# Kernel tuning notes

Hardware: AMD Instinct MI355X
Metric: run time of the kernel (lower is better)

Reference implementation:

```python
import jax, jax.numpy as jnp
import numpy as np

B, N, C, H = 8, 4096, 768, 32
D = C // H  # head_dim = 24
EPS = 1e-12


def _l2norm(t):
    # F.normalize(dim=-1): t / max(||t||_2, eps)
    n = jnp.sqrt(jnp.sum(t * t, axis=-1, keepdims=True))
    return t / jnp.maximum(n, EPS)


def setup_inputs() -> dict:
    key = jax.random.key(0)
    ks = jax.random.split(key, 6)
    s_in = 1.0 / np.sqrt(C)
    return {
        "x": jax.random.normal(ks[0], (B, N, C), dtype=jnp.float32),
        "W_qkv": jax.random.uniform(ks[1], (C, 3 * C), jnp.float32, -s_in, s_in),
        "b_qkv": jax.random.uniform(ks[2], (3 * C,), jnp.float32, -s_in, s_in),
        "temperature": jnp.ones((H, 1, 1), dtype=jnp.float32),
        "W_proj": jax.random.uniform(ks[3], (C, C), jnp.float32, -s_in, s_in),
        "b_proj": jax.random.uniform(ks[4], (C,), jnp.float32, -s_in, s_in),
    }


def reference(x, W_qkv, b_qkv, temperature, W_proj, b_proj):
    b, n, c = x.shape
    qkv = x @ W_qkv + b_qkv                                  # (B,N,3C)
    qkv = qkv.reshape(b, n, 3, H, D).transpose(2, 0, 3, 1, 4)  # (3,B,H,N,D)
    q, k, v = qkv[0], qkv[1], qkv[2]                         # (B,H,N,D)
    q = jnp.swapaxes(q, -1, -2)                              # (B,H,D,N)
    k = jnp.swapaxes(k, -1, -2)
    v = jnp.swapaxes(v, -1, -2)
    q = _l2norm(q)                                           # normalize over N
    k = _l2norm(k)
    attn = jnp.einsum('bhdn,bhen->bhde', q, k) * temperature  # (B,H,D,D)
    attn = jax.nn.softmax(attn, axis=-1)
    y = jnp.einsum('bhde,bhen->bhdn', attn, v)               # (B,H,D,N)
    # Faithful to torch: (1,B,H,D,N).transpose(1,2).reshape(B,N,C)
    # == (H,B,D,N) flattened row-major into (B,N,C)
    y = jnp.transpose(y, (1, 0, 2, 3)).reshape(b, n, c)
    return y @ W_proj + b_proj
```

## Files before the change

### kernel.cpp

```cpp
#include <hip/hip_runtime.h>
#include <hip/hip_bf16.h>


#define DEVI __device__ __forceinline__

typedef __attribute__((ext_vector_type(8))) short bf16x8;
typedef __attribute__((ext_vector_type(4))) float f32x4;
typedef __attribute__((ext_vector_type(4))) unsigned int u32x4;
typedef unsigned int u32;
typedef unsigned short u16;

DEVI u16 f2bf(float f) {
  union { float f; u32 u; } x; x.f = f;
  u32 r = x.u + 0x7FFFu + ((x.u >> 16) & 1u);
  return (u16)(r >> 16);
}

DEVI u32 cvtpk(float a, float b) {
  u32 r;
  asm("v_cvt_pk_bf16_f32 %0, %1, %2" : "=v"(r) : "v"(a), "v"(b));
  return r;
}

DEVI void gload_lds16(const void* g, void* l) {
  __builtin_amdgcn_global_load_lds((__attribute__((address_space(1))) void*)g,
                                   (__attribute__((address_space(3))) void*)l, 16, 0, 0);
}

__global__ __launch_bounds__(256) void transpose_cvt(const float* __restrict__ W,
                                                     u16* __restrict__ Wt, int K, int N) {
  __shared__ float tile[32][33];
  int n0 = blockIdx.x * 32, k0 = blockIdx.y * 32;
  int tx = threadIdx.x, ty = threadIdx.y;
  #pragma unroll
  for (int i = 0; i < 4; ++i)
    tile[ty + 8 * i][tx] = W[(long)(k0 + ty + 8 * i) * N + n0 + tx];
  __syncthreads();
  #pragma unroll
  for (int i = 0; i < 4; ++i)
    Wt[(long)(n0 + ty + 8 * i) * K + k0 + tx] = f2bf(tile[tx][ty + 8 * i]);
}

template<int NT>
__global__ __launch_bounds__(512, 2) void gemm_k1f_kernel(
    const float* __restrict__ X, const u16* __restrict__ Bt,
    const float* __restrict__ bias, u16* __restrict__ Cout, int N) {
  constexpr int K = NT * 32;
  __shared__ __attribute__((aligned(128))) char lds[73728];

  int nbx = N >> 8;
  int nwg = gridDim.x;
  int bid = blockIdx.x;
  bid = (bid & 7) * (nwg >> 3) + (bid >> 3);
  int bx = bid % nbx, by = bid / nbx;

  int t = threadIdx.x;
  int w = t >> 6, l = t & 63;
  int wr = w >> 2, wc = w & 3;
  int l16 = l & 15, l4 = l >> 4;

  int cbb = (l4 * 16) ^ ((l16 & 8) << 2);
  int pA0 = (wr * 64 + l16) * 64 + cbb;
  int pB0 = (wc * 64 + l16) * 64 + cbb;

  int pa = t * 16;
  int la = pa ^ (((pa >> 9) & 1) << 5);
  int soffA = (la >> 6) * K + ((la & 63) >> 1);
  int soffB[2];
  #pragma unroll
  for (int j = 0; j < 2; ++j) {
    int p = (j * 512 + t) * 16;
    int lb = p ^ (((p >> 9) & 1) << 5);
    soffB[j] = (lb >> 6) * K + ((lb & 63) >> 1);
  }

  const float* Ag = X + (long)by * 128 * K;
  const u16* Bg = Bt + (long)bx * 256 * K;
  int sdst = w * 1024;

  f32x4 acc[4][4] = {};
  f32x4 rC0, rC1, rN0, rN1;

  rC0 = *(const f32x4*)(Ag + soffA);
  rC1 = *(const f32x4*)(Ag + soffA + 4);
  #pragma unroll
  for (int j = 0; j < 2; ++j)
    gload_lds16(Bg + soffB[j], lds + 24576 + j * 8192 + sdst);
  rN0 = *(const f32x4*)(Ag + soffA + 32);
  rN1 = *(const f32x4*)(Ag + soffA + 36);
  #pragma unroll
  for (int j = 0; j < 2; ++j)
    gload_lds16(Bg + soffB[j] + 32, lds + 24576 + 16384 + j * 8192 + sdst);
  asm volatile("s_waitcnt vmcnt(6)" ::: "memory");
  {
    u32x4 wv;
    wv[0] = cvtpk(rC0[0], rC0[1]); wv[1] = cvtpk(rC0[2], rC0[3]);
    wv[2] = cvtpk(rC1[0], rC1[1]); wv[3] = cvtpk(rC1[2], rC1[3]);
    *(u32x4*)(lds + t * 16) = wv;
  }
  rC0 = rN0; rC1 = rN1;

  #pragma unroll
  for (int kt = 0; kt < NT; ++kt) {
    int rs = kt % 3;
    if (kt + 2 < NT) {
      rN0 = *(const f32x4*)(Ag + soffA + (kt + 2) * 32);
      rN1 = *(const f32x4*)(Ag + soffA + (kt + 2) * 32 + 4);
      #pragma unroll
      for (int j = 0; j < 2; ++j)
        gload_lds16(Bg + soffB[j] + (kt + 2) * 32,
                    lds + 24576 + ((kt + 2) % 3) * 16384 + j * 8192 + sdst);
      asm volatile("s_waitcnt vmcnt(4)" ::: "memory");
    } else if (kt + 2 == NT) {
      asm volatile("s_waitcnt vmcnt(2)" ::: "memory");
    } else {
      asm volatile("s_waitcnt vmcnt(0)" ::: "memory");
    }
    if (kt + 1 < NT) {
      u32x4 wv;
      wv[0] = cvtpk(rC0[0], rC0[1]); wv[1] = cvtpk(rC0[2], rC0[3]);
      wv[2] = cvtpk(rC1[0], rC1[1]); wv[3] = cvtpk(rC1[2], rC1[3]);
      *(u32x4*)(lds + ((kt + 1) % 3) * 8192 + t * 16) = wv;
      rC0 = rN0; rC1 = rN1;
    }
    asm volatile("s_waitcnt lgkmcnt(0)" ::: "memory");
    __builtin_amdgcn_sched_barrier(0);
    __builtin_amdgcn_s_barrier();
    __builtin_amdgcn_sched_barrier(0);

    bf16x8 aF[4], bF[4];
    #pragma unroll
    for (int mi = 0; mi < 4; ++mi)
      aF[mi] = *(const bf16x8*)(lds + rs * 8192 + mi * 1024 + pA0);
    #pragma unroll
    for (int n = 0; n < 4; ++n)
      bF[n] = *(const bf16x8*)(lds + 24576 + rs * 16384 + n * 1024 + pB0);

    __builtin_amdgcn_s_setprio(1);
    #pragma unroll
    for (int mi = 0; mi < 4; ++mi)
      #pragma unroll
      for (int n = 0; n < 4; ++n)
        acc[mi][n] = __builtin_amdgcn_mfma_f32_16x16x32_bf16(aF[mi], bF[n], acc[mi][n], 0, 0, 0);
    __builtin_amdgcn_s_setprio(0);
    __builtin_amdgcn_s_barrier();
    __builtin_amdgcn_sched_barrier(0);
  }

  #pragma unroll
  for (int mi = 0; mi < 4; ++mi) {
    int row0 = by * 128 + wr * 64 + mi * 16 + l4 * 4;
    #pragma unroll
    for (int n = 0; n < 4; ++n) {
      int col = bx * 256 + wc * 64 + n * 16 + l16;
      float bv = bias[col];
      #pragma unroll
      for (int j = 0; j < 4; ++j) {
        long idx = (long)(row0 + j) * N + col;
        Cout[idx] = f2bf(acc[mi][n][j] + bv);
      }
    }
  }
}

#define STAGE3(ktile, slot)                                                    \
  { _Pragma("unroll") for (int j_ = 0; j_ < 2; ++j_) {                         \
      gload_lds16(Ag + soffA[j_] + (ktile) * 32,                               \
                  lds + (slot) * 8192 + j_ * 4096 + sdst);                     \
      gload_lds16(Bg + soffB[j_] + (ktile) * 32,                               \
                  lds + 24576 + (slot) * 8192 + j_ * 4096 + sdst); } }

template<int NT>
__global__ __launch_bounds__(256, 3) void gemm3c_kernel(
    const u16* __restrict__ A, const u16* __restrict__ Bt,
    const float* __restrict__ bias, float* __restrict__ Cout,
    int M, int N) {
  constexpr int K = NT * 32;
  __shared__ __attribute__((aligned(128))) char lds[49152];

  int nbx = N >> 7;
  int nwg = gridDim.x;
  int bid = blockIdx.x;
  bid = (bid & 7) * (nwg >> 3) + (bid >> 3);
  int bx = bid % nbx, by = bid / nbx;

  int t = threadIdx.x;
  int w = t >> 6, l = t & 63;
  int wr = w >> 1, wc = w & 1;
  int l16 = l & 15, l4 = l >> 4;

  int cbb = (l4 * 16) ^ ((l16 & 8) << 2);
  int pA0 = (wr * 64 + l16) * 64 + cbb;
  int pB0 = (wc * 64 + l16) * 64 + cbb;

  int soffA[2], soffB[2];
  #pragma unroll
  for (int j = 0; j < 2; ++j) {
    int p = (j * 256 + t) * 16;
    int lb = p ^ (((p >> 9) & 1) << 5);
    soffA[j] = (lb >> 6) * K + ((lb & 63) >> 1);
    soffB[j] = soffA[j];
  }

  const u16* Ag = A + (long)by * 128 * K;
  const u16* Bg = Bt + (long)bx * 128 * K;
  int sdst = w * 1024;

  f32x4 acc[4][4] = {};

  STAGE3(0, 0);
  STAGE3(1, 1);

  #pragma unroll
  for (int kt = 0; kt < NT; ++kt) {
    int rs = kt % 3;
    if (kt + 2 < NT) {
      STAGE3(kt + 2, (kt + 2) % 3);
      asm volatile("s_waitcnt vmcnt(8)" ::: "memory");
    } else if (kt + 2 == NT) {
      asm volatile("s_waitcnt vmcnt(4)" ::: "memory");
    } else {
      asm volatile("s_waitcnt vmcnt(0)" ::: "memory");
    }
    __builtin_amdgcn_sched_barrier(0);
    __builtin_amdgcn_s_barrier();
    __builtin_amdgcn_sched_barrier(0);

    bf16x8 aF[4], bF[4];
    #pragma unroll
    for (int mi = 0; mi < 4; ++mi)
      aF[mi] = *(const bf16x8*)(lds + rs * 8192 + mi * 1024 + pA0);
    #pragma unroll
    for (int n = 0; n < 4; ++n)
      bF[n] = *(const bf16x8*)(lds + 24576 + rs * 8192 + n * 1024 + pB0);

    __builtin_amdgcn_s_setprio(1);
    #pragma unroll
    for (int mi = 0; mi < 4; ++mi)
      #pragma unroll
      for (int n = 0; n < 4; ++n)
        acc[mi][n] = __builtin_amdgcn_mfma_f32_16x16x32_bf16(aF[mi], bF[n], acc[mi][n], 0, 0, 0);
    __builtin_amdgcn_s_setprio(0);
    __builtin_amdgcn_s_barrier();
    __builtin_amdgcn_sched_barrier(0);
  }

  #pragma unroll
  for (int mi = 0; mi < 4; ++mi) {
    int row0 = by * 128 + wr * 64 + mi * 16 + l4 * 4;
    #pragma unroll
    for (int n = 0; n < 4; ++n) {
      int col = bx * 128 + wc * 64 + n * 16 + l16;
      float bv = bias[col];
      #pragma unroll
      for (int j = 0; j < 4; ++j) {
        long idx = (long)(row0 + j) * N + col;
        __builtin_nontemporal_store(acc[mi][n][j] + bv, Cout + idx);
      }
    }
  }
}

#define PFQK(nc, rq, rk)                                                       \
  { long cb = (long)(nc) * 589824;                                             \
    _Pragma("unroll") for (int i = 0; i < 3; ++i) {                            \
      rq[i] = *(const uint4*)(qbase + cb + offI[i]);                           \
      rk[i] = *(const uint4*)(kbase + cb + offI[i]); } }

#define WRQK(rq, rk)                                                           \
  { _Pragma("unroll") for (int i = 0; i < 3; ++i) {                            \
      const u32* pq = (const u32*)&rq[i];                                      \
      const u32* pk = (const u32*)&rk[i];                                      \
      _Pragma("unroll") for (int j = 0; j < 4; ++j) {                          \
        int d = sI[i] * 8 + 2 * j;                                             \
        qt[d][nI[i]] = (u16)pq[j]; qt[d + 1][nI[i]] = (u16)(pq[j] >> 16);      \
        kt[d][nI[i]] = (u16)pk[j]; kt[d + 1][nI[i]] = (u16)(pk[j] >> 16); } } }

#define GRAM8                                                                  \
  { _Pragma("unroll") for (int ks = 0; ks < 8; ++ks) {                         \
      int koff = ks * 32 + l4 * 8;                                             \
      bf16x8 qa = *(const bf16x8*)&qt[fm * 16 + l16][koff];                    \
      bf16x8 qb = *(const bf16x8*)&qt[fn * 16 + l16][koff];                    \
      bf16x8 ka = *(const bf16x8*)&kt[fm * 16 + l16][koff];                    \
      bf16x8 kb = *(const bf16x8*)&kt[fn * 16 + l16][koff];                    \
      accG = __builtin_amdgcn_mfma_f32_16x16x32_bf16(qa, kb, accG, 0, 0, 0);   \
      accQ = __builtin_amdgcn_mfma_f32_16x16x32_bf16(qa, qb, accQ, 0, 0, 0);   \
      accK = __builtin_amdgcn_mfma_f32_16x16x32_bf16(ka, kb, accK, 0, 0, 0); } }

__global__ __launch_bounds__(256) void gram_kernel(const u16* __restrict__ qkv,
                                                   float* __restrict__ gram) {
  __shared__ u16 qt[32][280];
  __shared__ u16 kt[32][280];

  int bid = blockIdx.x;
  int bh = bid >> 2, s = bid & 3;
  int b = bh >> 5, h = bh & 31;
  int t = threadIdx.x;
  int w = t >> 6, l = t & 63;
  int l16 = l & 15, l4 = l >> 4;
  int fm = w >> 1, fn = w & 1;

  for (int i = t; i < 32 * 280; i += 256) { qt[0][i] = 0; kt[0][i] = 0; }

  int nI[3], sI[3], offI[3];
  #pragma unroll
  for (int i = 0; i < 3; ++i) {
    int idx = t + 256 * i;
    nI[i] = idx / 3; sI[i] = idx % 3;
    offI[i] = nI[i] * 2304 + sI[i] * 8;
  }

  f32x4 accG = {}, accQ = {}, accK = {};
  const u16* qbase = qkv + (long)b * 4096 * 2304 + h * 24;
  const u16* kbase = qbase + 768;
  int c0 = s * 4;

  uint4 rq[3], rk[3];
  PFQK(c0, rq, rk);
  __syncthreads();

  #pragma unroll
  for (int c = 0; c < 4; ++c) {
    WRQK(rq, rk);
    __syncthreads();
    if (c + 1 < 4) PFQK(c0 + c + 1, rq, rk);
    GRAM8;
    __syncthreads();
  }

  float* gb = gram + (long)(bh * 4 + s) * 3072;
  int row = fm * 16 + l4 * 4, col = fn * 16 + l16;
  #pragma unroll
  for (int j = 0; j < 4; ++j) {
    gb[(row + j) * 32 + col] = accG[j];
    gb[1024 + (row + j) * 32 + col] = accQ[j];
    gb[2048 + (row + j) * 32 + col] = accK[j];
  }
}

__global__ __launch_bounds__(32) void softmax_kernel(const float* __restrict__ gram,
                                                     const float* __restrict__ temperature,
                                                     u16* __restrict__ attnb) {
  int bh = blockIdx.x;
  int h = bh & 31;
  int d = threadIdx.x;
  u16* ab = attnb + bh * 1024;
  if (d < 24) {
    const float* gb = gram + (long)bh * 12288;
    float nq2 = 0.f, row[24], nk2[24];
    #pragma unroll
    for (int e = 0; e < 24; ++e) { row[e] = 0.f; nk2[e] = 0.f; }
    #pragma unroll
    for (int s = 0; s < 4; ++s) {
      const float* gs = gb + s * 3072;
      nq2 += gs[1024 + d * 33];
      #pragma unroll
      for (int e = 0; e < 24; ++e) {
        row[e] += gs[d * 32 + e];
        nk2[e] += gs[2048 + e * 33];
      }
    }
    float nq = fmaxf(sqrtf(fmaxf(nq2, 0.f)), 1e-12f);
    float tmp = temperature[h];
    float mx = -1e30f;
    #pragma unroll
    for (int e = 0; e < 24; ++e) {
      float nk = fmaxf(sqrtf(fmaxf(nk2[e], 0.f)), 1e-12f);
      row[e] = row[e] / (nq * nk) * tmp;
      mx = fmaxf(mx, row[e]);
    }
    float ssum = 0.f;
    #pragma unroll
    for (int e = 0; e < 24; ++e) { row[e] = __expf(row[e] - mx); ssum += row[e]; }
    float inv = 1.f / ssum;
    #pragma unroll
    for (int e = 0; e < 24; ++e) ab[d * 32 + e] = f2bf(row[e] * inv);
    #pragma unroll
    for (int e = 24; e < 32; ++e) ab[d * 32 + e] = 0;
  } else {
    #pragma unroll
    for (int e = 0; e < 32; ++e) ab[d * 32 + e] = 0;
  }
}

__global__ __launch_bounds__(256) void pv_kernel(const u16* __restrict__ qkv,
                                                 const u16* __restrict__ attnb,
                                                 u16* __restrict__ yout) {
  __shared__ u16 vl[256][40];
  int bid = blockIdx.x;
  int bh = bid >> 4, c = bid & 15;
  int b = bh >> 5, h = bh & 31;
  int t = threadIdx.x;
  int w = t >> 6, l = t & 63;
  int l16 = l & 15, l4 = l >> 4;

  for (int i = t; i < 5120; i += 256) ((u32*)vl)[i] = 0;

  const u16* ab = attnb + bh * 1024;
  bf16x8 af0 = *(const bf16x8*)(ab + l16 * 32 + l4 * 8);
  bf16x8 af1 = *(const bf16x8*)(ab + (16 + l16) * 32 + l4 * 8);

  const u16* vbase = qkv + (long)b * 4096 * 2304 + h * 24 + 1536;
  uint4 rv[3];
  int nI[3], sI[3];
  #pragma unroll
  for (int i = 0; i < 3; ++i) {
    int idx = t + 256 * i;
    nI[i] = idx / 3; sI[i] = idx % 3;
    rv[i] = *(const uint4*)(vbase + (long)c * 589824 + nI[i] * 2304 + sI[i] * 8);
  }
  __syncthreads();
  #pragma unroll
  for (int i = 0; i < 3; ++i) *(uint4*)&vl[nI[i]][sI[i] * 8] = rv[i];
  __syncthreads();

  u16* ybase = yout + (long)(h * 8 + b) * 24 * 4096;
  int n0 = c * 256;
  f32x4 z = {};
  #pragma unroll
  for (int fnn = 0; fnn < 4; ++fnn) {
    int ncol = w * 64 + fnn * 16 + l16;
    bf16x8 bv = *(const bf16x8*)&vl[ncol][l4 * 8];
    f32x4 y0 = __builtin_amdgcn_mfma_f32_16x16x32_bf16(af0, bv, z, 0, 0, 0);
    f32x4 y1 = __builtin_amdgcn_mfma_f32_16x16x32_bf16(af1, bv, z, 0, 0, 0);
    int gn = n0 + ncol;
    #pragma unroll
    for (int j = 0; j < 4; ++j) {
      int d0 = l4 * 4 + j;
      ybase[(long)d0 * 4096 + gn] = f2bf(y0[j]);
      int d1 = 16 + d0;
      if (d1 < 24) ybase[(long)d1 * 4096 + gn] = f2bf(y1[j]);
    }
  }
}

extern "C" void kernel_launch(void* const* d_in, const int* in_sizes, int n_in,
                              void* d_out, int out_size, void* d_ws, size_t ws_size,
                              hipStream_t stream) {
  const float* x     = (const float*)d_in[0];
  const float* Wqkv  = (const float*)d_in[1];
  const float* bqkv  = (const float*)d_in[2];
  const float* temp  = (const float*)d_in[3];
  const float* Wproj = (const float*)d_in[4];
  const float* bproj = (const float*)d_in[5];
  float* out = (float*)d_out;

  char* ws = (char*)d_ws;
  float* gram  = (float*)(ws);
  u16*   y     = (u16*)(ws);
  u16*   wqt   = (u16*)(ws + 50331648);
  u16*   attnb = (u16*)(ws + 50331648);
  u16*   wpt   = (u16*)(ws + 53870592);
  u16*   qkv   = (u16*)(ws + 55050240);

  transpose_cvt<<<dim3(72, 24), dim3(32, 8), 0, stream>>>(Wqkv, wqt, 768, 2304);
  transpose_cvt<<<dim3(24, 24), dim3(32, 8), 0, stream>>>(Wproj, wpt, 768, 768);
  gemm_k1f_kernel<24><<<2304, 512, 0, stream>>>(x, wqt, bqkv, qkv, 2304);
  gram_kernel<<<1024, 256, 0, stream>>>(qkv, gram);
  softmax_kernel<<<256, 32, 0, stream>>>(gram, temp, attnb);
  pv_kernel<<<4096, 256, 0, stream>>>(qkv, attnb, y);
  gemm3c_kernel<24><<<1536, 256, 0, stream>>>(y, wpt, bproj, out, 32768, 768);
}
```

Measured before the change: 329.3 us.

## Pre-convert x to bf16 and use 4-wave 64x128 warp tiles in QKV GEMM

Adds a separate kernel that converts x from fp32 to bf16 in workspace, so the QKV GEMM can stage both A and B tiles directly into LDS with global_load_lds. The in-loop register load, convert and LDS store are removed. The GEMM also drops from 8 waves to 4 waves per block, each computing a 64x128 tile with 32 accumulators, which gives more MFMA reuse per LDS fragment. In exchange, x now makes an extra round trip through memory (a 100MB read plus a 50MB write), and the larger accumulator set raises register pressure.

```diff
diff --git a/kernel.cpp b/kernel.cpp
--- a/kernel.cpp
+++ b/kernel.cpp
@@ -6,7 +6,6 @@
 
 typedef __attribute__((ext_vector_type(8))) short bf16x8;
 typedef __attribute__((ext_vector_type(4))) float f32x4;
-typedef __attribute__((ext_vector_type(4))) unsigned int u32x4;
 typedef unsigned int u32;
 typedef unsigned short u16;
 
@@ -16,15 +15,24 @@
   return (u16)(r >> 16);
 }
 
-DEVI u32 cvtpk(float a, float b) {
-  u32 r;
-  asm("v_cvt_pk_bf16_f32 %0, %1, %2" : "=v"(r) : "v"(a), "v"(b));
-  return r;
-}
-
 DEVI void gload_lds16(const void* g, void* l) {
   __builtin_amdgcn_global_load_lds((__attribute__((address_space(1))) void*)g,
                                    (__attribute__((address_space(3))) void*)l, 16, 0, 0);
+}
+
+__global__ __launch_bounds__(256) void cvt_kernel(const float* __restrict__ in,
+                                                  u16* __restrict__ out, int n8) {
+  int i = blockIdx.x * 256 + threadIdx.x;
+  if (i >= n8) return;
+  long o = (long)i * 8;
+  float4 a = *(const float4*)(in + o);
+  float4 b = *(const float4*)(in + o + 4);
+  uint4 v;
+  v.x = f2bf(a.x) | ((u32)f2bf(a.y) << 16);
+  v.y = f2bf(a.z) | ((u32)f2bf(a.w) << 16);
+  v.z = f2bf(b.x) | ((u32)f2bf(b.y) << 16);
+  v.w = f2bf(b.z) | ((u32)f2bf(b.w) << 16);
+  *(uint4*)(out + o) = v;
 }
 
 __global__ __launch_bounds__(256) void transpose_cvt(const float* __restrict__ W,
@@ -42,8 +50,8 @@
 }
 
 template<int NT>
-__global__ __launch_bounds__(512, 2) void gemm_k1f_kernel(
-    const float* __restrict__ X, const u16* __restrict__ Bt,
+__global__ __launch_bounds__(256, 2) void gemm_w1_kernel(
+    const u16* __restrict__ A, const u16* __restrict__ Bt,
     const float* __restrict__ bias, u16* __restrict__ Cout, int N) {
   constexpr int K = NT * 32;
   __shared__ __attribute__((aligned(128))) char lds[73728];
@@ -56,91 +64,72 @@
 
   int t = threadIdx.x;
   int w = t >> 6, l = t & 63;
-  int wr = w >> 2, wc = w & 3;
+  int wr = w >> 1, wc = w & 1;
   int l16 = l & 15, l4 = l >> 4;
 
   int cbb = (l4 * 16) ^ ((l16 & 8) << 2);
   int pA0 = (wr * 64 + l16) * 64 + cbb;
-  int pB0 = (wc * 64 + l16) * 64 + cbb;
-
-  int pa = t * 16;
-  int la = pa ^ (((pa >> 9) & 1) << 5);
-  int soffA = (la >> 6) * K + ((la & 63) >> 1);
-  int soffB[2];
+  int pB0 = (wc * 128 + l16) * 64 + cbb;
+
+  int soffA[2], soffB[4];
   #pragma unroll
   for (int j = 0; j < 2; ++j) {
-    int p = (j * 512 + t) * 16;
+    int p = (j * 256 + t) * 16;
+    int la = p ^ (((p >> 9) & 1) << 5);
+    soffA[j] = (la >> 6) * K + ((la & 63) >> 1);
+  }
+  #pragma unroll
+  for (int j = 0; j < 4; ++j) {
+    int p = (j * 256 + t) * 16;
     int lb = p ^ (((p >> 9) & 1) << 5);
     soffB[j] = (lb >> 6) * K + ((lb & 63) >> 1);
   }
 
-  const float* Ag = X + (long)by * 128 * K;
+  const u16* Ag = A + (long)by * 128 * K;
   const u16* Bg = Bt + (long)bx * 256 * K;
   int sdst = w * 1024;
 
-  f32x4 acc[4][4] = {};
-  f32x4 rC0, rC1, rN0, rN1;
-
-  rC0 = *(const f32x4*)(Ag + soffA);
-  rC1 = *(const f32x4*)(Ag + soffA + 4);
-  #pragma unroll
-  for (int j = 0; j < 2; ++j)
-    gload_lds16(Bg + soffB[j], lds + 24576 + j * 8192 + sdst);
-  rN0 = *(const f32x4*)(Ag + soffA + 32);
-  rN1 = *(const f32x4*)(Ag + soffA + 36);
-  #pragma unroll
-  for (int j = 0; j < 2; ++j)
-    gload_lds16(Bg + soffB[j] + 32, lds + 24576 + 16384 + j * 8192 + sdst);
-  asm volatile("s_waitcnt vmcnt(6)" ::: "memory");
-  {
-    u32x4 wv;
-    wv[0] = cvtpk(rC0[0], rC0[1]); wv[1] = cvtpk(rC0[2], rC0[3]);
-    wv[2] = cvtpk(rC1[0], rC1[1]); wv[3] = cvtpk(rC1[2], rC1[3]);
-    *(u32x4*)(lds + t * 16) = wv;
-  }
-  rC0 = rN0; rC1 = rN1;
+  f32x4 acc[4][8] = {};
+
+#define STAGE_W1(ktile, slot)                                                  \
+  { _Pragma("unroll") for (int j_ = 0; j_ < 2; ++j_)                           \
+      gload_lds16(Ag + soffA[j_] + (ktile) * 32,                               \
+                  lds + (slot) * 8192 + j_ * 4096 + sdst);                     \
+    _Pragma("unroll") for (int j_ = 0; j_ < 4; ++j_)                           \
+      gload_lds16(Bg + soffB[j_] + (ktile) * 32,                               \
+                  lds + 24576 + (slot) * 16384 + j_ * 4096 + sdst); }
+
+  STAGE_W1(0, 0);
+  STAGE_W1(1, 1);
 
   #pragma unroll
   for (int kt = 0; kt < NT; ++kt) {
     int rs = kt % 3;
     if (kt + 2 < NT) {
-      rN0 = *(const f32x4*)(Ag + soffA + (kt + 2) * 32);
-      rN1 = *(const f32x4*)(Ag + soffA + (kt + 2) * 32 + 4);
-      #pragma unroll
-      for (int j = 0; j < 2; ++j)
-        gload_lds16(Bg + soffB[j] + (kt + 2) * 32,
-                    lds + 24576 + ((kt + 2) % 3) * 16384 + j * 8192 + sdst);
-      asm volatile("s_waitcnt vmcnt(4)" ::: "memory");
+      STAGE_W1(kt + 2, (kt + 2) % 3);
+      asm volatile("s_waitcnt vmcnt(12)" ::: "memory");
     } else if (kt + 2 == NT) {
-      asm volatile("s_waitcnt vmcnt(2)" ::: "memory");
+      asm volatile("s_waitcnt vmcnt(6)" ::: "memory");
     } else {
       asm volatile("s_waitcnt vmcnt(0)" ::: "memory");
     }
-    if (kt + 1 < NT) {
-      u32x4 wv;
-      wv[0] = cvtpk(rC0[0], rC0[1]); wv[1] = cvtpk(rC0[2], rC0[3]);
-      wv[2] = cvtpk(rC1[0], rC1[1]); wv[3] = cvtpk(rC1[2], rC1[3]);
-      *(u32x4*)(lds + ((kt + 1) % 3) * 8192 + t * 16) = wv;
-      rC0 = rN0; rC1 = rN1;
-    }
-    asm volatile("s_waitcnt lgkmcnt(0)" ::: "memory");
     __builtin_amdgcn_sched_barrier(0);
     __builtin_amdgcn_s_barrier();
     __builtin_amdgcn_sched_barrier(0);
 
-    bf16x8 aF[4], bF[4];
+    bf16x8 aF[4], bF[8];
     #pragma unroll
     for (int mi = 0; mi < 4; ++mi)
       aF[mi] = *(const bf16x8*)(lds + rs * 8192 + mi * 1024 + pA0);
     #pragma unroll
-    for (int n = 0; n < 4; ++n)
+    for (int n = 0; n < 8; ++n)
       bF[n] = *(const bf16x8*)(lds + 24576 + rs * 16384 + n * 1024 + pB0);
 
     __builtin_amdgcn_s_setprio(1);
     #pragma unroll
     for (int mi = 0; mi < 4; ++mi)
       #pragma unroll
-      for (int n = 0; n < 4; ++n)
+      for (int n = 0; n < 8; ++n)
         acc[mi][n] = __builtin_amdgcn_mfma_f32_16x16x32_bf16(aF[mi], bF[n], acc[mi][n], 0, 0, 0);
     __builtin_amdgcn_s_setprio(0);
     __builtin_amdgcn_s_barrier();
@@ -151,8 +140,8 @@
   for (int mi = 0; mi < 4; ++mi) {
     int row0 = by * 128 + wr * 64 + mi * 16 + l4 * 4;
     #pragma unroll
-    for (int n = 0; n < 4; ++n) {
-      int col = bx * 256 + wc * 64 + n * 16 + l16;
+    for (int n = 0; n < 8; ++n) {
+      int col = bx * 256 + wc * 128 + n * 16 + l16;
       float bv = bias[col];
       #pragma unroll
       for (int j = 0; j < 4; ++j) {
@@ -161,6 +150,7 @@
       }
     }
   }
+#undef STAGE_W1
 }
 
 #define STAGE3(ktile, slot)                                                    \
@@ -446,6 +436,7 @@
   float* out = (float*)d_out;
 
   char* ws = (char*)d_ws;
+  u16*   xb    = (u16*)(ws);
   float* gram  = (float*)(ws);
   u16*   y     = (u16*)(ws);
   u16*   wqt   = (u16*)(ws + 50331648);
@@ -453,9 +444,10 @@
   u16*   wpt   = (u16*)(ws + 53870592);
   u16*   qkv   = (u16*)(ws + 55050240);
 
+  cvt_kernel<<<12288, 256, 0, stream>>>(x, xb, 3145728);
   transpose_cvt<<<dim3(72, 24), dim3(32, 8), 0, stream>>>(Wqkv, wqt, 768, 2304);
   transpose_cvt<<<dim3(24, 24), dim3(32, 8), 0, stream>>>(Wproj, wpt, 768, 768);
-  gemm_k1f_kernel<24><<<2304, 512, 0, stream>>>(x, wqt, bqkv, qkv, 2304);
+  gemm_w1_kernel<24><<<2304, 256, 0, stream>>>(xb, wqt, bqkv, qkv, 2304);
   gram_kernel<<<1024, 256, 0, stream>>>(qkv, gram);
   softmax_kernel<<<256, 32, 0, stream>>>(gram, temp, attnb);
   pv_kernel<<<4096, 256, 0, stream>>>(qkv, attnb, y);
```

Result: faster. 295.7 us (-10.2%).
